# Kernel optimization log

Hardware: AMD Instinct MI355X
Metric: run time of the kernel (lower is better)

Reference implementation:

```python
import jax, jax.numpy as jnp
import numpy as np
import math

B, S, D, H, DH = 1, 2048, 2048, 16, 64  # batch, seq, d_model, n_heads, d_head
LAMBDA_INIT = 0.8
EPS = 1e-5


def setup_inputs() -> dict:
    key = jax.random.key(0)
    ks = jax.random.split(key, 10)
    w_scale = 0.02
    inner = 2 * DH * H  # == D here
    return {
        "x": jax.random.normal(ks[0], (B, S, D), dtype=jnp.float32),
        "Wq": jax.random.normal(ks[1], (D, inner), dtype=jnp.float32) * w_scale,
        "Wk": jax.random.normal(ks[2], (D, inner), dtype=jnp.float32) * w_scale,
        "Wv": jax.random.normal(ks[3], (D, inner), dtype=jnp.float32) * w_scale,
        "Wo": jax.random.normal(ks[4], (inner, D), dtype=jnp.float32) * w_scale,
        "lambda_q1": jax.random.normal(ks[5], (DH,), dtype=jnp.float32) * 0.1,
        "lambda_k1": jax.random.normal(ks[6], (DH,), dtype=jnp.float32) * 0.1,
        "lambda_q2": jax.random.normal(ks[7], (DH,), dtype=jnp.float32) * 0.1,
        "lambda_k2": jax.random.normal(ks[8], (DH,), dtype=jnp.float32) * 0.1,
        "gn_weight": jnp.ones((inner,), dtype=jnp.float32),
        "gn_bias": jnp.zeros((inner,), dtype=jnp.float32),
    }


def reference(x, Wq, Wk, Wv, Wo, lambda_q1, lambda_k1, lambda_q2, lambda_k2,
              gn_weight, gn_bias):
    b, s, _ = x.shape
    dh = lambda_q1.shape[0]
    h = Wq.shape[1] // (2 * dh)
    scale = 1.0 / math.sqrt(dh)

    q = (x @ Wq).reshape(b, s, h, 2, dh)
    k = (x @ Wk).reshape(b, s, h, 2, dh)
    v = (x @ Wv).reshape(b, s, h, 2 * dh)

    # [B,H,S,dh]
    q1 = jnp.swapaxes(q[..., 0, :], 1, 2)
    q2 = jnp.swapaxes(q[..., 1, :], 1, 2)
    k1 = jnp.swapaxes(k[..., 0, :], 1, 2)
    k2 = jnp.swapaxes(k[..., 1, :], 1, 2)
    vh = jnp.swapaxes(v, 1, 2)  # [B,H,S,2*dh]

    score1 = jnp.einsum("bhsd,bhtd->bhst", q1, k1) * scale
    score2 = jnp.einsum("bhsd,bhtd->bhst", q2, k2) * scale
    attn1 = jax.nn.softmax(score1, axis=-1)
    attn2 = jax.nn.softmax(score2, axis=-1)

    lam = (jnp.exp(jnp.sum(lambda_q1 * lambda_k1))
           - jnp.exp(jnp.sum(lambda_q2 * lambda_k2)) + LAMBDA_INIT)

    out = jnp.einsum("bhst,bhtd->bhsd", attn1 - lam * attn2, vh)  # [B,H,S,2dh]
    out = jnp.swapaxes(out, 1, 2)  # [B,S,H,2dh]

    # GroupNorm: n_heads groups over the channel dim, per token
    mu = jnp.mean(out, axis=-1, keepdims=True)
    var = jnp.var(out, axis=-1, keepdims=True)
    out = (out - mu) * jax.lax.rsqrt(var + EPS)
    gw = gn_weight.reshape(h, 2 * dh)
    gb = gn_bias.reshape(h, 2 * dh)
    out = out * gw + gb

    out = out * (1.0 - LAMBDA_INIT)
    return out.reshape(b, s, -1) @ Wo
```

## Files before the change

### kernel.cpp

```cpp
#include <hip/hip_runtime.h>
#include <hip/hip_bf16.h>

typedef unsigned short u16;
typedef __attribute__((ext_vector_type(8))) short short8;
typedef __attribute__((ext_vector_type(4))) short short4v;
typedef __attribute__((ext_vector_type(4))) float f32x4;

#define S_DIM 2048
#define D_DIM 2048
#define H_NUM 16
#define DH_NUM 64

__device__ __forceinline__ u16 f2bf(float f) {
    union { float f; unsigned u; } x; x.f = f;
    unsigned r = x.u + 0x7fff + ((x.u >> 16) & 1);
    return (u16)(r >> 16);
}

__device__ __forceinline__ void gload16(const void* g, void* l) {
    __builtin_amdgcn_global_load_lds(
        (const __attribute__((address_space(1))) unsigned int*)g,
        (__attribute__((address_space(3))) unsigned int*)l, 16, 0, 0);
}

__global__ __launch_bounds__(256)
void cvt_bf16(const float* __restrict__ src, u16* __restrict__ dst)
{
    int i = (blockIdx.x * 256 + threadIdx.x) * 4;
    float4 v = *(const float4*)(src + i);
    ushort4 o;
    o.x = f2bf(v.x); o.y = f2bf(v.y); o.z = f2bf(v.z); o.w = f2bf(v.w);
    *(ushort4*)(dst + i) = o;
}

__global__ __launch_bounds__(256)
void transpose_w(const float* __restrict__ src, u16* __restrict__ dst)
{
    __shared__ __attribute__((aligned(16))) u16 tile[64][65];
    const int tx = threadIdx.x & 63, ty = threadIdx.x >> 6;
    const int bx = blockIdx.x * 64, by = blockIdx.y * 64;
    for (int i = ty; i < 64; i += 4)
        tile[i][tx] = f2bf(src[(by + i) * D_DIM + bx + tx]);
    __syncthreads();
    for (int i = ty; i < 64; i += 4)
        dst[(bx + i) * D_DIM + by + tx] = tile[tx][i];
}

__global__ __launch_bounds__(256, 2)
void gemm128(const u16* __restrict__ A,
             const u16* B0, const u16* B1, const u16* B2,
             u16* C0, u16* C1, u16* C2, int zbase)
{
    const int Kd = D_DIM, N = D_DIM, M = S_DIM;
    const int z = blockIdx.z + zbase;
    const u16* Bt = (z == 0) ? B0 : (z == 1) ? B1 : B2;
    u16* C        = (z == 0) ? C0 : (z == 1) ? C1 : C2;

    __shared__ __attribute__((aligned(16))) u16 As[128 * 32];
    __shared__ __attribute__((aligned(16))) u16 Bs[128 * 32];

    const int tid = threadIdx.x, lane = tid & 63, wave = tid >> 6;
    const int bm = blockIdx.x * 128, bn = blockIdx.y * 128;

    const int lrow = lane >> 2;
    const int gchunk = (lane & 3) ^ ((lane >> 3) & 3);
    const long aoff0 = (long)(bm + wave * 32 + lrow) * Kd + gchunk * 8;
    const long aoff1 = aoff0 + 16L * Kd;
    const long boff0 = (long)(bn + wave * 32 + lrow) * Kd + gchunk * 8;
    const long boff1 = boff0 + 16L * Kd;
    u16* as0 = &As[wave * 1024];
    u16* as1 = &As[wave * 1024 + 512];
    u16* bs0 = &Bs[wave * 1024];
    u16* bs1 = &Bs[wave * 1024 + 512];

    const int wr = (wave >> 1) * 64, wc = (wave & 1) * 64;
    const int fr = lane & 15, fq = lane >> 4;

    f32x4 acc[4][4];
    for (int i = 0; i < 4; ++i)
        for (int j = 0; j < 4; ++j) { f32x4 zz = {0.f,0.f,0.f,0.f}; acc[i][j] = zz; }

    for (int k0 = 0; k0 < Kd; k0 += 32) {
        gload16(A + aoff0 + k0, as0);
        gload16(A + aoff1 + k0, as1);
        gload16(Bt + boff0 + k0, bs0);
        gload16(Bt + boff1 + k0, bs1);
        __syncthreads();

        short8 af[4], bf[4];
#pragma unroll
        for (int i = 0; i < 4; ++i) {
            int m = wr + i * 16 + fr;
            int slot = fq ^ ((m >> 1) & 3);
            af[i] = *(const short8*)&As[m * 32 + slot * 8];
            int n = wc + i * 16 + fr;
            int slotb = fq ^ ((n >> 1) & 3);
            bf[i] = *(const short8*)&Bs[n * 32 + slotb * 8];
        }
#pragma unroll
        for (int i = 0; i < 4; ++i)
#pragma unroll
            for (int j = 0; j < 4; ++j)
                acc[i][j] = __builtin_amdgcn_mfma_f32_16x16x32_bf16(af[i], bf[j], acc[i][j], 0, 0, 0);
        __syncthreads();
    }

    const float sc = (z == 0) ? 0.125f : 1.0f;
#pragma unroll
    for (int i = 0; i < 4; ++i) {
        int row = bm + wr + i * 16 + fq * 4;
#pragma unroll
        for (int j = 0; j < 4; ++j) {
            int col = bn + wc + j * 16 + fr;
#pragma unroll
            for (int r = 0; r < 4; ++r) {
                u16 v = f2bf(acc[i][j][r] * sc);
                if (z == 2) C[(long)col * M + (row + r)] = v;
                else        C[(long)(row + r) * N + col] = v;
            }
        }
    }
}

__global__ __launch_bounds__(256, 2)
void gemm_out(const u16* __restrict__ A, const u16* __restrict__ Bt,
              float* __restrict__ C)
{
    const int Kd = D_DIM, N = D_DIM;

    __shared__ __attribute__((aligned(16))) u16 As[64 * 32];
    __shared__ __attribute__((aligned(16))) u16 Bs[128 * 32];

    const int tid = threadIdx.x, lane = tid & 63, wave = tid >> 6;
    const int bm = blockIdx.x * 64, bn = blockIdx.y * 128;

    const int lrow = lane >> 2;
    const int gchunk = (lane & 3) ^ ((lane >> 3) & 3);
    const long aoff  = (long)(bm + wave * 16 + lrow) * Kd + gchunk * 8;
    const long boff0 = (long)(bn + wave * 32 + lrow) * Kd + gchunk * 8;
    const long boff1 = boff0 + 16L * Kd;
    u16* as  = &As[wave * 512];
    u16* bs0 = &Bs[wave * 1024];
    u16* bs1 = &Bs[wave * 1024 + 512];

    const int wr = (wave >> 1) * 32, wc = (wave & 1) * 64;
    const int fr = lane & 15, fq = lane >> 4;

    f32x4 acc[2][4];
    for (int i = 0; i < 2; ++i)
        for (int j = 0; j < 4; ++j) { f32x4 zz = {0.f,0.f,0.f,0.f}; acc[i][j] = zz; }

    for (int k0 = 0; k0 < Kd; k0 += 32) {
        gload16(A + aoff + k0, as);
        gload16(Bt + boff0 + k0, bs0);
        gload16(Bt + boff1 + k0, bs1);
        __syncthreads();

        short8 af[2], bf[4];
#pragma unroll
        for (int i = 0; i < 2; ++i) {
            int m = wr + i * 16 + fr;
            int slot = fq ^ ((m >> 1) & 3);
            af[i] = *(const short8*)&As[m * 32 + slot * 8];
        }
#pragma unroll
        for (int j = 0; j < 4; ++j) {
            int n = wc + j * 16 + fr;
            int slotb = fq ^ ((n >> 1) & 3);
            bf[j] = *(const short8*)&Bs[n * 32 + slotb * 8];
        }
#pragma unroll
        for (int i = 0; i < 2; ++i)
#pragma unroll
            for (int j = 0; j < 4; ++j)
                acc[i][j] = __builtin_amdgcn_mfma_f32_16x16x32_bf16(af[i], bf[j], acc[i][j], 0, 0, 0);
        __syncthreads();
    }

#pragma unroll
    for (int i = 0; i < 2; ++i) {
        int row = bm + wr + i * 16 + fq * 4;
#pragma unroll
        for (int j = 0; j < 4; ++j) {
            int col = bn + wc + j * 16 + fr;
#pragma unroll
            for (int r = 0; r < 4; ++r)
                C[(long)(row + r) * N + col] = acc[i][j][r];
        }
    }
}

__global__ __launch_bounds__(256, 2)
void diff_attn(const u16* __restrict__ Qm, const u16* __restrict__ Km,
               const u16* __restrict__ Vt,
               const float* __restrict__ lq1, const float* __restrict__ lk1,
               const float* __restrict__ lq2, const float* __restrict__ lk2,
               const float* __restrict__ gw, const float* __restrict__ gb,
               u16* __restrict__ Y)
{
    __shared__ __attribute__((aligned(16))) u16 K1s[64 * 72];
    __shared__ __attribute__((aligned(16))) u16 K2s[64 * 72];
    __shared__ __attribute__((aligned(16))) u16 Vts[128 * 72];

    const int tid = threadIdx.x, lane = tid & 63, wave = tid >> 6;
    const int h = blockIdx.y;
    const int q0 = blockIdx.x * 64 + wave * 16;
    const int fr = lane & 15, qq = lane >> 4;

    float d1 = 0.f, d2 = 0.f;
    for (int i = 0; i < DH_NUM; ++i) {
        d1 += lq1[i] * lk1[i];
        d2 += lq2[i] * lk2[i];
    }
    const float lam = __expf(d1) - __expf(d2) + 0.8f;

    short8 q1f[2], q2f[2];
    {
        const u16* qb = Qm + (long)(q0 + fr) * D_DIM + h * 128;
        q1f[0] = *(const short8*)(qb + qq * 8);
        q1f[1] = *(const short8*)(qb + 32 + qq * 8);
        q2f[0] = *(const short8*)(qb + 64 + qq * 8);
        q2f[1] = *(const short8*)(qb + 96 + qq * 8);
    }

    f32x4 a1[8], a2[8];
    for (int n = 0; n < 8; ++n) { f32x4 zz = {0.f,0.f,0.f,0.f}; a1[n] = zz; a2[n] = zz; }
    float ls1 = 0.f, ls2 = 0.f;

    for (int kb = 0; kb < S_DIM / 64; ++kb) {
        __syncthreads();
        {
            const long krow = (long)(kb * 64) * D_DIM + h * 128;
#pragma unroll
            for (int it = 0; it < 2; ++it) {
                int idx = tid + it * 256;
                int t = idx >> 3, c = idx & 7;
                *(short8*)&K1s[t * 72 + c * 8] =
                    *(const short8*)&Km[krow + (long)t * D_DIM + c * 8];
                *(short8*)&K2s[t * 72 + c * 8] =
                    *(const short8*)&Km[krow + (long)t * D_DIM + 64 + c * 8];
            }
#pragma unroll
            for (int it = 0; it < 4; ++it) {
                int idx = tid + it * 256;
                int rr = idx >> 3, c = idx & 7;
                *(short8*)&Vts[rr * 72 + c * 8] =
                    *(const short8*)&Vt[(long)(h * 128 + rr) * S_DIM + kb * 64 + c * 8];
            }
        }
        __syncthreads();

#pragma unroll
        for (int j = 0; j < 4; ++j) {
            f32x4 s1 = {0.f,0.f,0.f,0.f}, s2 = {0.f,0.f,0.f,0.f};
#pragma unroll
            for (int ks = 0; ks < 2; ++ks) {
                short8 k1 = *(const short8*)&K1s[(j * 16 + fr) * 72 + ks * 32 + qq * 8];
                short8 k2 = *(const short8*)&K2s[(j * 16 + fr) * 72 + ks * 32 + qq * 8];
                s1 = __builtin_amdgcn_mfma_f32_16x16x32_bf16(k1, q1f[ks], s1, 0, 0, 0);
                s2 = __builtin_amdgcn_mfma_f32_16x16x32_bf16(k2, q2f[ks], s2, 0, 0, 0);
            }
            short4v p1, p2;
#pragma unroll
            for (int r = 0; r < 4; ++r) {
                float e1 = __expf(s1[r]);
                float e2 = __expf(s2[r]);
                ls1 += e1; ls2 += e2;
                p1[r] = (short)f2bf(e1);
                p2[r] = (short)f2bf(e2);
            }
#pragma unroll
            for (int n = 0; n < 8; ++n) {
                short4v vf = *(const short4v*)&Vts[(n * 16 + fr) * 72 + j * 16 + qq * 4];
                a1[n] = __builtin_amdgcn_mfma_f32_16x16x16bf16_1k(vf, p1, a1[n], 0, 0, 0);
                a2[n] = __builtin_amdgcn_mfma_f32_16x16x16bf16_1k(vf, p2, a2[n], 0, 0, 0);
            }
        }
    }

    float L1 = ls1, L2 = ls2;
    L1 += __shfl_xor(L1, 16, 64); L1 += __shfl_xor(L1, 32, 64);
    L2 += __shfl_xor(L2, 16, 64); L2 += __shfl_xor(L2, 32, 64);
    const float i1 = 1.f / L1, i2 = lam / L2;

    float o[8][4], sum = 0.f, sq = 0.f;
#pragma unroll
    for (int n = 0; n < 8; ++n)
#pragma unroll
        for (int r = 0; r < 4; ++r) {
            float v = a1[n][r] * i1 - a2[n][r] * i2;
            o[n][r] = v; sum += v; sq += v * v;
        }
    sum += __shfl_xor(sum, 16, 64); sum += __shfl_xor(sum, 32, 64);
    sq  += __shfl_xor(sq, 16, 64);  sq  += __shfl_xor(sq, 32, 64);
    const float mean = sum * (1.f / 128.f);
    const float var = sq * (1.f / 128.f) - mean * mean;
    const float inv = rsqrtf(var + 1e-5f);

    const long yrow = (long)(q0 + fr) * D_DIM + h * 128;
#pragma unroll
    for (int n = 0; n < 8; ++n) {
        float4 g4 = *(const float4*)&gw[h * 128 + n * 16 + qq * 4];
        float4 b4 = *(const float4*)&gb[h * 128 + n * 16 + qq * 4];
        ushort4 st;
        st.x = f2bf(((o[n][0] - mean) * inv * g4.x + b4.x) * 0.2f);
        st.y = f2bf(((o[n][1] - mean) * inv * g4.y + b4.y) * 0.2f);
        st.z = f2bf(((o[n][2] - mean) * inv * g4.z + b4.z) * 0.2f);
        st.w = f2bf(((o[n][3] - mean) * inv * g4.w + b4.w) * 0.2f);
        *(ushort4*)&Y[yrow + n * 16 + qq * 4] = st;
    }
}

extern "C" void kernel_launch(void* const* d_in, const int* in_sizes, int n_in,
                              void* d_out, int out_size, void* d_ws, size_t ws_size,
                              hipStream_t stream)
{
    const float* x   = (const float*)d_in[0];
    const float* Wq  = (const float*)d_in[1];
    const float* Wk  = (const float*)d_in[2];
    const float* Wv  = (const float*)d_in[3];
    const float* Wo  = (const float*)d_in[4];
    const float* lq1 = (const float*)d_in[5];
    const float* lk1 = (const float*)d_in[6];
    const float* lq2 = (const float*)d_in[7];
    const float* lk2 = (const float*)d_in[8];
    const float* gw  = (const float*)d_in[9];
    const float* gb  = (const float*)d_in[10];

    char* ws = (char*)d_ws;
    const size_t SEG = (size_t)D_DIM * D_DIM * sizeof(u16);
    const dim3 tgrid(32, 32), agrid(32, 16), ogrid(32, 16);

    if (ws_size >= 7 * SEG) {
        u16* XB  = (u16*)(ws + 0 * SEG);
        u16* WTq = (u16*)(ws + 1 * SEG);
        u16* WTk = (u16*)(ws + 2 * SEG);
        u16* WTv = (u16*)(ws + 3 * SEG);
        u16* Qb  = (u16*)(ws + 4 * SEG);
        u16* Kb  = (u16*)(ws + 5 * SEG);
        u16* Vt  = (u16*)(ws + 6 * SEG);
        u16* Yb  = WTq;
        u16* WTo = WTk;

        cvt_bf16<<<4096, 256, 0, stream>>>(x, XB);
        transpose_w<<<tgrid, 256, 0, stream>>>(Wq, WTq);
        transpose_w<<<tgrid, 256, 0, stream>>>(Wk, WTk);
        transpose_w<<<tgrid, 256, 0, stream>>>(Wv, WTv);
        gemm128<<<dim3(16, 16, 3), 256, 0, stream>>>(XB, WTq, WTk, WTv,
                                                     Qb, Kb, Vt, 0);
        diff_attn<<<agrid, 256, 0, stream>>>(Qb, Kb, Vt, lq1, lk1, lq2, lk2,
                                             gw, gb, Yb);
        transpose_w<<<tgrid, 256, 0, stream>>>(Wo, WTo);
        gemm_out<<<ogrid, 256, 0, stream>>>(Yb, WTo, (float*)d_out);
    } else {
        u16* XB = (u16*)(ws + 0 * SEG);
        u16* WT = (u16*)(ws + 1 * SEG);
        u16* Qb = (u16*)(ws + 2 * SEG);
        u16* Kb = (u16*)(ws + 3 * SEG);
        u16* Vt = (u16*)(ws + 4 * SEG);

        cvt_bf16<<<4096, 256, 0, stream>>>(x, XB);
        transpose_w<<<tgrid, 256, 0, stream>>>(Wq, WT);
        gemm128<<<dim3(16, 16, 1), 256, 0, stream>>>(XB, WT, WT, WT, Qb, Qb, Qb, 0);
        transpose_w<<<tgrid, 256, 0, stream>>>(Wk, WT);
        gemm128<<<dim3(16, 16, 1), 256, 0, stream>>>(XB, WT, WT, WT, Kb, Kb, Kb, 1);
        transpose_w<<<tgrid, 256, 0, stream>>>(Wv, WT);
        gemm128<<<dim3(16, 16, 1), 256, 0, stream>>>(XB, WT, WT, WT, Vt, Vt, Vt, 2);
        diff_attn<<<agrid, 256, 0, stream>>>(Qb, Kb, Vt, lq1, lk1, lq2, lk2,
                                             gw, gb, XB);
        transpose_w<<<tgrid, 256, 0, stream>>>(Wo, WT);
        gemm_out<<<ogrid, 256, 0, stream>>>(XB, WT, (float*)d_out);
    }
}
```

Baseline: 334.8 us.

## Double-buffer K/V tiles in diff_attn with register prefetch of next tile

The attention kernel now keeps two LDS buffers for the K1/K2/Vt tiles. It issues global loads for the next key block into registers before computing on the current block, then writes them to the alternate buffer afterwards. This drops one __syncthreads per iteration and is meant to hide global load latency behind the MFMA work. In exchange it doubles LDS use (about 36 KB per block) and adds 8 short8 registers per thread, which may reduce occupancy under launch_bounds(256,2).

```diff
diff --git a/kernel.cpp b/kernel.cpp
--- a/kernel.cpp
+++ b/kernel.cpp
@@ -198,9 +198,9 @@
                const float* __restrict__ gw, const float* __restrict__ gb,
                u16* __restrict__ Y)
 {
-    __shared__ __attribute__((aligned(16))) u16 K1s[64 * 72];
-    __shared__ __attribute__((aligned(16))) u16 K2s[64 * 72];
-    __shared__ __attribute__((aligned(16))) u16 Vts[128 * 72];
+    __shared__ __attribute__((aligned(16))) u16 K1s[2][64 * 72];
+    __shared__ __attribute__((aligned(16))) u16 K2s[2][64 * 72];
+    __shared__ __attribute__((aligned(16))) u16 Vts[2][128 * 72];
 
     const int tid = threadIdx.x, lane = tid & 63, wave = tid >> 6;
     const int h = blockIdx.y;
@@ -227,36 +227,45 @@
     for (int n = 0; n < 8; ++n) { f32x4 zz = {0.f,0.f,0.f,0.f}; a1[n] = zz; a2[n] = zz; }
     float ls1 = 0.f, ls2 = 0.f;
 
+    const int t0 = tid >> 3, c0 = tid & 7;
+    short8 k1r[2], k2r[2], vr[4];
+
+    auto load_tile = [&](int kb) {
+        const long krow = (long)(kb * 64) * D_DIM + h * 128;
+        k1r[0] = *(const short8*)&Km[krow + (long)t0 * D_DIM + c0 * 8];
+        k2r[0] = *(const short8*)&Km[krow + (long)t0 * D_DIM + 64 + c0 * 8];
+        k1r[1] = *(const short8*)&Km[krow + (long)(t0 + 32) * D_DIM + c0 * 8];
+        k2r[1] = *(const short8*)&Km[krow + (long)(t0 + 32) * D_DIM + 64 + c0 * 8];
+#pragma unroll
+        for (int it = 0; it < 4; ++it)
+            vr[it] = *(const short8*)&Vt[(long)(h * 128 + t0 + it * 32) * S_DIM + kb * 64 + c0 * 8];
+    };
+    auto store_tile = [&](int b) {
+        *(short8*)&K1s[b][t0 * 72 + c0 * 8] = k1r[0];
+        *(short8*)&K2s[b][t0 * 72 + c0 * 8] = k2r[0];
+        *(short8*)&K1s[b][(t0 + 32) * 72 + c0 * 8] = k1r[1];
+        *(short8*)&K2s[b][(t0 + 32) * 72 + c0 * 8] = k2r[1];
+#pragma unroll
+        for (int it = 0; it < 4; ++it)
+            *(short8*)&Vts[b][(t0 + it * 32) * 72 + c0 * 8] = vr[it];
+    };
+
+    load_tile(0);
+    store_tile(0);
+    int p = 0;
+
     for (int kb = 0; kb < S_DIM / 64; ++kb) {
         __syncthreads();
-        {
-            const long krow = (long)(kb * 64) * D_DIM + h * 128;
-#pragma unroll
-            for (int it = 0; it < 2; ++it) {
-                int idx = tid + it * 256;
-                int t = idx >> 3, c = idx & 7;
-                *(short8*)&K1s[t * 72 + c * 8] =
-                    *(const short8*)&Km[krow + (long)t * D_DIM + c * 8];
-                *(short8*)&K2s[t * 72 + c * 8] =
-                    *(const short8*)&Km[krow + (long)t * D_DIM + 64 + c * 8];
-            }
-#pragma unroll
-            for (int it = 0; it < 4; ++it) {
-                int idx = tid + it * 256;
-                int rr = idx >> 3, c = idx & 7;
-                *(short8*)&Vts[rr * 72 + c * 8] =
-                    *(const short8*)&Vt[(long)(h * 128 + rr) * S_DIM + kb * 64 + c * 8];
-            }
-        }
-        __syncthreads();
+        const bool more = (kb + 1 < S_DIM / 64);
+        if (more) load_tile(kb + 1);
 
 #pragma unroll
         for (int j = 0; j < 4; ++j) {
             f32x4 s1 = {0.f,0.f,0.f,0.f}, s2 = {0.f,0.f,0.f,0.f};
 #pragma unroll
             for (int ks = 0; ks < 2; ++ks) {
-                short8 k1 = *(const short8*)&K1s[(j * 16 + fr) * 72 + ks * 32 + qq * 8];
-                short8 k2 = *(const short8*)&K2s[(j * 16 + fr) * 72 + ks * 32 + qq * 8];
+                short8 k1 = *(const short8*)&K1s[p][(j * 16 + fr) * 72 + ks * 32 + qq * 8];
+                short8 k2 = *(const short8*)&K2s[p][(j * 16 + fr) * 72 + ks * 32 + qq * 8];
                 s1 = __builtin_amdgcn_mfma_f32_16x16x32_bf16(k1, q1f[ks], s1, 0, 0, 0);
                 s2 = __builtin_amdgcn_mfma_f32_16x16x32_bf16(k2, q2f[ks], s2, 0, 0, 0);
             }
@@ -271,11 +280,14 @@
             }
 #pragma unroll
             for (int n = 0; n < 8; ++n) {
-                short4v vf = *(const short4v*)&Vts[(n * 16 + fr) * 72 + j * 16 + qq * 4];
+                short4v vf = *(const short4v*)&Vts[p][(n * 16 + fr) * 72 + j * 16 + qq * 4];
                 a1[n] = __builtin_amdgcn_mfma_f32_16x16x16bf16_1k(vf, p1, a1[n], 0, 0, 0);
                 a2[n] = __builtin_amdgcn_mfma_f32_16x16x16bf16_1k(vf, p2, a2[n], 0, 0, 0);
             }
         }
+
+        if (more) store_tile(p ^ 1);
+        p ^= 1;
     }
 
     float L1 = ls1, L2 = ls2;
```

Result: no change. 328.8 us (-1.8%).
